# Kernel optimization log

Hardware: AMD Instinct MI355X
Metric: run time of the kernel (lower is better)

Reference implementation:

```python
import jax, jax.numpy as jnp
import numpy as np

DIM = 128
NUM_SLOTS = 8
ITERS = 3
EPS = 1e-8
LN_EPS = 1e-3
HIDDEN = max(DIM, 128)


def _ln(x, w, b):
    mu = jnp.mean(x, axis=-1, keepdims=True)
    var = jnp.mean(jnp.square(x - mu), axis=-1, keepdims=True)
    return (x - mu) * jax.lax.rsqrt(var + LN_EPS) * w + b


def setup_inputs() -> dict:
    key = jax.random.key(0)
    ks = jax.random.split(key, 16)
    b, n, d, h = 32, 4096, DIM, HIDDEN
    limit = np.sqrt(6.0 / (1 + d))
    inp = {
        'inputs': jax.random.normal(ks[0], (b, n, d), jnp.float32),
        'slots_mu': jax.random.uniform(ks[1], (1, 1, d), jnp.float32, -limit, limit),
        'slots_log_sigma': jax.random.uniform(ks[2], (1, 1, d), jnp.float32, -limit, limit),
        'Wq': jax.random.normal(ks[3], (d, d), jnp.float32) / np.sqrt(d),
        'Wk': jax.random.normal(ks[4], (d, d), jnp.float32) / np.sqrt(d),
        'Wv': jax.random.normal(ks[5], (d, d), jnp.float32) / np.sqrt(d),
        'W_ih': jax.random.normal(ks[6], (3 * d, d), jnp.float32) / np.sqrt(d),
        'W_hh': jax.random.normal(ks[7], (3 * d, d), jnp.float32) / np.sqrt(d),
        'b_ih': jnp.zeros((3 * d,), jnp.float32),
        'b_hh': jnp.zeros((3 * d,), jnp.float32),
        'W1': jax.random.normal(ks[8], (h, d), jnp.float32) / np.sqrt(d),
        'b1': jnp.zeros((h,), jnp.float32),
        'W2': jax.random.normal(ks[9], (d, h), jnp.float32) / np.sqrt(h),
        'b2': jnp.zeros((d,), jnp.float32),
        'ln_in_w': jnp.ones((d,), jnp.float32), 'ln_in_b': jnp.zeros((d,), jnp.float32),
        'ln_s_w': jnp.ones((d,), jnp.float32), 'ln_s_b': jnp.zeros((d,), jnp.float32),
        'ln_ff_w': jnp.ones((d,), jnp.float32), 'ln_ff_b': jnp.zeros((d,), jnp.float32),
    }
    return inp


def reference(inputs, slots_mu, slots_log_sigma, Wq, Wk, Wv, W_ih, W_hh, b_ih, b_hh,
              W1, b1, W2, b2, ln_in_w, ln_in_b, ln_s_w, ln_s_b, ln_ff_w, ln_ff_b):
    b, n, d = inputs.shape
    scale = d ** -0.5
    # stochastic slot init (reparameterized, fixed key for determinism)
    noise = jax.random.normal(jax.random.key(42), (b, NUM_SLOTS, d), inputs.dtype)
    slots = slots_mu + jnp.exp(slots_log_sigma) * noise

    x = _ln(inputs, ln_in_w, ln_in_b)
    k = jnp.einsum('bnd,ed->bne', x, Wk)
    v = jnp.einsum('bnd,ed->bne', x, Wv)

    for _ in range(ITERS):
        slots_prev = slots
        q = jnp.einsum('bsd,ed->bse', _ln(slots, ln_s_w, ln_s_b), Wq)
        dots = jnp.einsum('bid,bjd->bij', q, k) * scale          # [b, slots, n]
        attn = jax.nn.softmax(dots, axis=1) + EPS                 # softmax over slots
        attn = attn / jnp.sum(attn, axis=-1, keepdims=True)       # normalize over tokens
        updates = jnp.einsum('bjd,bij->bid', v, attn)             # [b, slots, d]
        # GRUCell(updates, slots_prev)
        gx = jnp.einsum('bsd,ed->bse', updates, W_ih) + b_ih
        gh = jnp.einsum('bsd,ed->bse', slots_prev, W_hh) + b_hh
        xr, xz, xn = jnp.split(gx, 3, axis=-1)
        hr, hz, hn = jnp.split(gh, 3, axis=-1)
        r = jax.nn.sigmoid(xr + hr)
        z = jax.nn.sigmoid(xz + hz)
        ng = jnp.tanh(xn + r * hn)
        slots = (1.0 - z) * ng + z * slots_prev
        # residual MLP
        ff = _ln(slots, ln_ff_w, ln_ff_b)
        ff = jax.nn.relu(jnp.einsum('bsd,hd->bsh', ff, W1) + b1)
        slots = slots + jnp.einsum('bsh,dh->bsd', ff, W2) + b2
    return slots
```

## Files before the change

kernel.cpp:

```cpp
#include <hip/hip_runtime.h>
#include <hip/hip_bf16.h>
#include <math.h>

#define DIM 128
#define NSLOT 8
#define NTOK 4096
#define NB 32
#define CHUNK 256
#define NCH (NTOK / CHUNK)
#define CHUNKPAD 264
#define LN_EPS 1e-3f
#define ATT_EPS 1e-8f
#define SCALE 0.08838834764831845f

#define BM 128
#define LDK 136

typedef short bf16x8 __attribute__((ext_vector_type(8)));
typedef float f32x4 __attribute__((ext_vector_type(4)));
typedef unsigned short ushort8_t __attribute__((ext_vector_type(8)));

__device__ __forceinline__ float bf2f(unsigned short u) {
  return __uint_as_float(((unsigned)u) << 16);
}
__device__ __forceinline__ unsigned short f2bf(float f) {
  unsigned u = __float_as_uint(f);
  unsigned r = (u + 0x7FFFu + ((u >> 16) & 1u)) >> 16;
  return (unsigned short)r;
}

__device__ __forceinline__ float erfinv_like_xla(float x) {
  double xd = (double)x;
  double w = -log1p(-xd * xd);
  double p;
  if (w < 5.0) {
    w = w - 2.5;
    p = 2.81022636e-08;
    p = 3.43273939e-07 + p * w;
    p = -3.5233877e-06 + p * w;
    p = -4.39150654e-06 + p * w;
    p = 0.00021858087 + p * w;
    p = -0.00125372503 + p * w;
    p = -0.00417768164 + p * w;
    p = 0.246640727 + p * w;
    p = 1.50140941 + p * w;
  } else {
    w = sqrt(w) - 3.0;
    p = -0.000200214257;
    p = 0.000100950558 + p * w;
    p = 0.00134934322 + p * w;
    p = -0.00367342844 + p * w;
    p = 0.00573950773 + p * w;
    p = -0.0076224613 + p * w;
    p = 0.00943887047 + p * w;
    p = 1.00167406 + p * w;
    p = 2.83297682 + p * w;
  }
  return (float)(p * xd);
}

__global__ __launch_bounds__(256) void k_init_slots(
    const float* __restrict__ mu, const float* __restrict__ lsig,
    float* __restrict__ slots) {
  int t = blockIdx.x * blockDim.x + threadIdx.x;
  if (t >= NB * NSLOT * DIM) return;
  uint32_t x0 = 0u, x1 = (uint32_t)t;
  uint32_t k0 = 0u, k1 = 42u;
  uint32_t ks[3] = {k0, k1, k0 ^ k1 ^ 0x1BD11BDAu};
  x0 += ks[0];
  x1 += ks[1];
  const int rot[2][4] = {{13, 15, 26, 6}, {17, 29, 16, 24}};
#pragma unroll
  for (int blk = 0; blk < 5; ++blk) {
    const int* r = rot[blk & 1];
#pragma unroll
    for (int j = 0; j < 4; ++j) {
      x0 += x1;
      x1 = (x1 << r[j]) | (x1 >> (32 - r[j]));
      x1 ^= x0;
    }
    x0 += ks[(blk + 1) % 3];
    x1 += ks[(blk + 2) % 3] + (uint32_t)(blk + 1);
  }
  uint32_t bits = x0 ^ x1;
  float f = __uint_as_float((bits >> 9) | 0x3F800000u) - 1.0f;
  const float mn = __uint_as_float(0xBF7FFFFFu);
  float u = fmaxf(f * 2.0f + mn, mn);
  float noise = 1.41421356f * erfinv_like_xla(u);
  int d = t & (DIM - 1);
  slots[t] = mu[d] + expf(lsig[d]) * noise;
}

__global__ __launch_bounds__(256) void k_wcast(const float* __restrict__ Wk,
                                               const float* __restrict__ Wv,
                                               unsigned short* __restrict__ Wbf) {
  int i = blockIdx.x * 256 + threadIdx.x;
  if (i >= DIM * DIM) return;
  Wbf[i] = f2bf(Wk[i]);
  Wbf[DIM * DIM + i] = f2bf(Wv[i]);
}

__global__ __launch_bounds__(512, 4) void k_ln_kv(
    const float* __restrict__ inp, const unsigned short* __restrict__ Wbf,
    const float* __restrict__ lnw, const float* __restrict__ lnb,
    unsigned short* __restrict__ kt, unsigned short* __restrict__ vt) {
  __shared__ __align__(16) unsigned short SH[BM * LDK];
  int t = threadIdx.x;
  int tg = blockIdx.x;

  {
    int r = t >> 2, qh = t & 3;
    const float* src = inp + ((size_t)tg * BM + r) * DIM + qh * 32;
    float xr[32];
    float s = 0.f, sq = 0.f;
#pragma unroll
    for (int i4 = 0; i4 < 8; ++i4) {
      float4 v = *reinterpret_cast<const float4*>(src + i4 * 4);
      xr[i4 * 4 + 0] = v.x; xr[i4 * 4 + 1] = v.y;
      xr[i4 * 4 + 2] = v.z; xr[i4 * 4 + 3] = v.w;
      s += v.x + v.y + v.z + v.w;
      sq += v.x * v.x + v.y * v.y + v.z * v.z + v.w * v.w;
    }
    s += __shfl_xor(s, 1); sq += __shfl_xor(sq, 1);
    s += __shfl_xor(s, 2); sq += __shfl_xor(sq, 2);
    float mean = s * (1.0f / DIM);
    float var = fmaxf(sq * (1.0f / DIM) - mean * mean, 0.0f);
    float inv = 1.0f / sqrtf(var + LN_EPS);
#pragma unroll
    for (int c8 = 0; c8 < 4; ++c8) {
      ushort8_t pk;
#pragma unroll
      for (int j = 0; j < 8; ++j) {
        int d = qh * 32 + c8 * 8 + j;
        float y = (xr[c8 * 8 + j] - mean) * inv * lnw[d] + lnb[d];
        pk[j] = f2bf(y);
      }
      *reinterpret_cast<ushort8_t*>(&SH[r * LDK + qh * 32 + c8 * 8]) = pk;
    }
  }
  __syncthreads();

  int w = t >> 6, l = t & 63, lm = l & 15, lg = l >> 4;
  int mat = w >> 2;
  int ebase = ((w >> 1) & 1) * 64;
  int th = (w & 1) * 64;
  const unsigned short* Wsrc = Wbf + mat * DIM * DIM;

  f32x4 acc[4][4];
#pragma unroll
  for (int i = 0; i < 4; ++i)
#pragma unroll
    for (int j = 0; j < 4; ++j) acc[i][j] = (f32x4){0.f, 0.f, 0.f, 0.f};

  if (mat == 0) {
#pragma unroll
    for (int ks = 0; ks < 4; ++ks) {
      bf16x8 wf[4], xf[4];
#pragma unroll
      for (int et = 0; et < 4; ++et)
        wf[et] = *reinterpret_cast<const bf16x8*>(
            Wsrc + (ebase + et * 16 + lm) * DIM + ks * 32 + 8 * lg);
#pragma unroll
      for (int tt = 0; tt < 4; ++tt)
        xf[tt] = *reinterpret_cast<const bf16x8*>(
            &SH[(th + tt * 16 + lm) * LDK + ks * 32 + 8 * lg]);
#pragma unroll
      for (int tt = 0; tt < 4; ++tt)
#pragma unroll
        for (int et = 0; et < 4; ++et)
          acc[tt][et] = __builtin_amdgcn_mfma_f32_16x16x32_bf16(
              xf[tt], wf[et], acc[tt][et], 0, 0, 0);
    }
  } else {
#pragma unroll
    for (int ks = 0; ks < 4; ++ks) {
      bf16x8 wf[4], xf[4];
#pragma unroll
      for (int et = 0; et < 4; ++et)
        wf[et] = *reinterpret_cast<const bf16x8*>(
            Wsrc + (ebase + et * 16 + lm) * DIM + ks * 32 + 8 * lg);
#pragma unroll
      for (int tt = 0; tt < 4; ++tt)
        xf[tt] = *reinterpret_cast<const bf16x8*>(
            &SH[(th + tt * 16 + lm) * LDK + ks * 32 + 8 * lg]);
#pragma unroll
      for (int et = 0; et < 4; ++et)
#pragma unroll
        for (int tt = 0; tt < 4; ++tt)
          acc[et][tt] = __builtin_amdgcn_mfma_f32_16x16x32_bf16(
              wf[et], xf[tt], acc[et][tt], 0, 0, 0);
    }
  }
  __syncthreads();

  if (mat == 0) {
#pragma unroll
    for (int tt = 0; tt < 4; ++tt)
#pragma unroll
      for (int et = 0; et < 4; ++et)
#pragma unroll
        for (int r = 0; r < 4; ++r)
          SH[(th + tt * 16 + 4 * lg + r) * LDK + ebase + et * 16 + lm] =
              f2bf(acc[tt][et][r]);
  }
  __syncthreads();
  {
    size_t rowbase = (size_t)tg * BM;
#pragma unroll
    for (int u = 0; u < 4; ++u) {
      int i = u * 512 + t;
      int tok = i >> 4, off = (i & 15) * 8;
      ushort8_t vv = *reinterpret_cast<const ushort8_t*>(&SH[tok * LDK + off]);
      *reinterpret_cast<ushort8_t*>(&kt[(rowbase + tok) * DIM + off]) = vv;
    }
  }
  __syncthreads();

  if (mat == 1) {
#pragma unroll
    for (int et = 0; et < 4; ++et)
#pragma unroll
      for (int tt = 0; tt < 4; ++tt)
#pragma unroll
        for (int r = 0; r < 4; ++r)
          SH[(ebase + et * 16 + 4 * lg + r) * LDK + th + tt * 16 + lm] =
              f2bf(acc[et][tt][r]);
  }
  __syncthreads();
  {
    int bb = tg >> 5;
    int nb = (tg & 31) * BM;
#pragma unroll
    for (int u = 0; u < 4; ++u) {
      int i = u * 512 + t;
      int e = i >> 4, off = (i & 15) * 8;
      ushort8_t vv = *reinterpret_cast<const ushort8_t*>(&SH[e * LDK + off]);
      *reinterpret_cast<ushort8_t*>(
          &vt[((size_t)bb * DIM + e) * NTOK + nb + off]) = vv;
    }
  }
}

__global__ __launch_bounds__(256) void k_q0(
    const float* __restrict__ slots, const float* __restrict__ Wq,
    const float* __restrict__ lnw, const float* __restrict__ lnb,
    unsigned short* __restrict__ qbf) {
  int b = blockIdx.x, t = threadIdx.x;
  int s = t >> 5, c = t & 31;
  __shared__ __align__(16) float sln[NSLOT][DIM];
  const float* sb = slots + (b * NSLOT + s) * DIM;
  float4 xv = *reinterpret_cast<const float4*>(sb + c * 4);
  float ps = xv.x + xv.y + xv.z + xv.w;
  float pq = xv.x * xv.x + xv.y * xv.y + xv.z * xv.z + xv.w * xv.w;
#pragma unroll
  for (int m = 16; m >= 1; m >>= 1) {
    ps += __shfl_xor(ps, m, 32);
    pq += __shfl_xor(pq, m, 32);
  }
  float mean = ps * (1.0f / DIM);
  float var = fmaxf(pq * (1.0f / DIM) - mean * mean, 0.0f);
  float inv = 1.0f / sqrtf(var + LN_EPS);
  float vals[4] = {xv.x, xv.y, xv.z, xv.w};
#pragma unroll
  for (int ii = 0; ii < 4; ++ii) {
    int d = c * 4 + ii;
    sln[s][d] = (vals[ii] - mean) * inv * lnw[d] + lnb[d];
  }
  __syncthreads();
#pragma unroll
  for (int ii = 0; ii < 4; ++ii) {
    int e = c + 32 * ii;
    const float* wr = Wq + e * DIM;
    float acc = 0.0f;
#pragma unroll
    for (int d4 = 0; d4 < DIM / 4; ++d4) {
      float4 w4 = *reinterpret_cast<const float4*>(wr + d4 * 4);
      float4 s4 = *reinterpret_cast<const float4*>(&sln[s][d4 * 4]);
      acc += s4.x * w4.x + s4.y * w4.y + s4.z * w4.z + s4.w * w4.w;
    }
    qbf[(b * NSLOT + s) * DIM + e] = f2bf(SCALE * acc);
  }
}

__global__ __launch_bounds__(512, 4) void k_attn(
    const unsigned short* __restrict__ qbf, const unsigned short* __restrict__ kt,
    const unsigned short* __restrict__ vt, float* __restrict__ Np,
    float* __restrict__ Dp) {
  int bid = blockIdx.x;
  int b = bid >> 4, ch = bid & 15;
  int n0 = ch * CHUNK;
  int t = threadIdx.x;
  int wid = t >> 6, l = t & 63, lm = l & 15, lg = l >> 4;

  __shared__ __align__(16) unsigned short a_lds[NSLOT][CHUNKPAD];

  {
    const unsigned short* qb = qbf + (b * NSLOT + (lm & 7)) * DIM;
    bf16x8 aq[4];
#pragma unroll
    for (int ks = 0; ks < 4; ++ks)
      aq[ks] = *reinterpret_cast<const bf16x8*>(qb + ks * 32 + 8 * lg);
    const unsigned short* kb = kt + ((size_t)b * NTOK + n0) * DIM;
#pragma unroll
    for (int tt = 0; tt < 2; ++tt) {
      int tok = wid * 32 + tt * 16 + lm;
      f32x4 acc = (f32x4){0.f, 0.f, 0.f, 0.f};
#pragma unroll
      for (int ks = 0; ks < 4; ++ks) {
        bf16x8 bk = *reinterpret_cast<const bf16x8*>(
            kb + (size_t)tok * DIM + ks * 32 + 8 * lg);
        acc = __builtin_amdgcn_mfma_f32_16x16x32_bf16(aq[ks], bk, acc, 0, 0, 0);
      }
      float m4 = fmaxf(fmaxf(acc[0], acc[1]), fmaxf(acc[2], acc[3]));
      float m8 = fmaxf(m4, __shfl_xor(m4, 16));
      float e0 = expf(acc[0] - m8), e1 = expf(acc[1] - m8);
      float e2 = expf(acc[2] - m8), e3 = expf(acc[3] - m8);
      float s4 = e0 + e1 + e2 + e3;
      float s8 = s4 + __shfl_xor(s4, 16);
      float rs = 1.0f / s8;
      if (lg < 2) {
        a_lds[4 * lg + 0][tok] = f2bf(e0 * rs + ATT_EPS);
        a_lds[4 * lg + 1][tok] = f2bf(e1 * rs + ATT_EPS);
        a_lds[4 * lg + 2][tok] = f2bf(e2 * rs + ATT_EPS);
        a_lds[4 * lg + 3][tok] = f2bf(e3 * rs + ATT_EPS);
      }
    }
  }
  __syncthreads();

  {
    float s = 0.0f;
#pragma unroll
    for (int jj = 0; jj < CHUNK / 64; ++jj) s += bf2f(a_lds[wid][l + 64 * jj]);
#pragma unroll
    for (int m = 32; m >= 1; m >>= 1) s += __shfl_xor(s, m);
    if (l == 0) Dp[(b * NCH + ch) * NSLOT + wid] = s;
  }

  {
    f32x4 acc = (f32x4){0.f, 0.f, 0.f, 0.f};
    const unsigned short* vb =
        vt + ((size_t)b * DIM + wid * 16 + lm) * NTOK + n0;
#pragma unroll
    for (int kk = 0; kk < CHUNK / 32; ++kk) {
      bf16x8 af = *reinterpret_cast<const bf16x8*>(
          &a_lds[lm & 7][kk * 32 + 8 * lg]);
      bf16x8 bv = *reinterpret_cast<const bf16x8*>(vb + kk * 32 + 8 * lg);
      acc = __builtin_amdgcn_mfma_f32_16x16x32_bf16(af, bv, acc, 0, 0, 0);
    }
    if (lg < 2) {
#pragma unroll
      for (int r = 0; r < 4; ++r)
        Np[((size_t)(b * NCH + ch) * NSLOT + 4 * lg + r) * DIM + wid * 16 +
           lm] = acc[r];
    }
  }
}

__global__ __launch_bounds__(256) void k_update(
    float* __restrict__ slots, unsigned short* __restrict__ qbf,
    const float* __restrict__ Np, const float* __restrict__ Dp,
    const float* __restrict__ W_ih, const float* __restrict__ W_hh,
    const float* __restrict__ b_ih, const float* __restrict__ b_hh,
    const float* __restrict__ W1, const float* __restrict__ b1,
    const float* __restrict__ W2, const float* __restrict__ b2,
    const float* __restrict__ lnfw, const float* __restrict__ lnfb,
    const float* __restrict__ Wq, const float* __restrict__ lnsw,
    const float* __restrict__ lnsb) {
  int bs = blockIdx.x;
  int b = bs >> 3, s = bs & 7;
  int t = threadIdx.x;
  __shared__ __align__(16) float upd[DIM];
  __shared__ __align__(16) float sprev[DIM];
  __shared__ __align__(16) float snew[DIM];
  __shared__ __align__(16) float ffin[DIM];
  __shared__ __align__(16) float ffb[DIM];
  __shared__ __align__(16) float gx[3 * DIM];
  __shared__ __align__(16) float gh[3 * DIM];

  float dsum = 0.0f;
  for (int ch = 0; ch < NCH; ++ch) dsum += Dp[(b * NCH + ch) * NSLOT + s];

  if (t < DIM) {
    sprev[t] = slots[(b * NSLOT + s) * DIM + t];
    float a = 0.0f;
    for (int ch = 0; ch < NCH; ++ch)
      a += Np[((size_t)(b * NCH + ch) * NSLOT + s) * DIM + t];
    upd[t] = a / dsum;
  }
  __syncthreads();

  for (int e = t; e < 3 * DIM; e += 256) {
    const float* wi = W_ih + e * DIM;
    const float* wh = W_hh + e * DIM;
    float ax = 0.0f, ah = 0.0f;
#pragma unroll
    for (int d4 = 0; d4 < DIM / 4; ++d4) {
      float4 u4 = *reinterpret_cast<const float4*>(&upd[d4 * 4]);
      float4 p4 = *reinterpret_cast<const float4*>(&sprev[d4 * 4]);
      float4 wi4 = *reinterpret_cast<const float4*>(wi + d4 * 4);
      float4 wh4 = *reinterpret_cast<const float4*>(wh + d4 * 4);
      ax += u4.x * wi4.x + u4.y * wi4.y + u4.z * wi4.z + u4.w * wi4.w;
      ah += p4.x * wh4.x + p4.y * wh4.y + p4.z * wh4.z + p4.w * wh4.w;
    }
    gx[e] = ax + b_ih[e];
    gh[e] = ah + b_hh[e];
  }
  __syncthreads();

  if (t < DIM) {
    float xr = gx[t], xz = gx[DIM + t], xn = gx[2 * DIM + t];
    float hr = gh[t], hz = gh[DIM + t], hn = gh[2 * DIM + t];
    float r = 1.0f / (1.0f + expf(-(xr + hr)));
    float z = 1.0f / (1.0f + expf(-(xz + hz)));
    float ng = tanhf(xn + r * hn);
    snew[t] = (1.0f - z) * ng + z * sprev[t];
  }
  __syncthreads();

  if (t < DIM) {
    float s1 = 0.0f, s2 = 0.0f;
#pragma unroll 8
    for (int d = 0; d < DIM; ++d) {
      float v = snew[d];
      s1 += v;
      s2 += v * v;
    }
    float mean = s1 * (1.0f / DIM);
    float var = fmaxf(s2 * (1.0f / DIM) - mean * mean, 0.0f);
    float inv = 1.0f / sqrtf(var + LN_EPS);
    ffin[t] = (snew[t] - mean) * inv * lnfw[t] + lnfb[t];
  }
  __syncthreads();

  if (t < DIM) {
    const float* wr = W1 + t * DIM;
    float acc = 0.0f;
#pragma unroll
    for (int d4 = 0; d4 < DIM / 4; ++d4) {
      float4 f4 = *reinterpret_cast<const float4*>(&ffin[d4 * 4]);
      float4 w4 = *reinterpret_cast<const float4*>(wr + d4 * 4);
      acc += f4.x * w4.x + f4.y * w4.y + f4.z * w4.z + f4.w * w4.w;
    }
    ffb[t] = fmaxf(acc + b1[t], 0.0f);
  }
  __syncthreads();

  if (t < DIM) {
    const float* wr = W2 + t * DIM;
    float acc = 0.0f;
#pragma unroll
    for (int h4 = 0; h4 < DIM / 4; ++h4) {
      float4 f4 = *reinterpret_cast<const float4*>(&ffb[h4 * 4]);
      float4 w4 = *reinterpret_cast<const float4*>(wr + h4 * 4);
      acc += f4.x * w4.x + f4.y * w4.y + f4.z * w4.z + f4.w * w4.w;
    }
    float val = snew[t] + acc + b2[t];
    slots[(b * NSLOT + s) * DIM + t] = val;
    gx[t] = val;
  }
  __syncthreads();

  if (t < DIM) {
    float s1 = 0.0f, s2 = 0.0f;
#pragma unroll 8
    for (int d = 0; d < DIM; ++d) {
      float v = gx[d];
      s1 += v;
      s2 += v * v;
    }
    float mean = s1 * (1.0f / DIM);
    float var = fmaxf(s2 * (1.0f / DIM) - mean * mean, 0.0f);
    float inv = 1.0f / sqrtf(var + LN_EPS);
    gh[t] = (gx[t] - mean) * inv * lnsw[t] + lnsb[t];
  }
  __syncthreads();

  if (t < DIM) {
    const float* wr = Wq + t * DIM;
    float acc = 0.0f;
#pragma unroll
    for (int d4 = 0; d4 < DIM / 4; ++d4) {
      float4 g4 = *reinterpret_cast<const float4*>(&gh[d4 * 4]);
      float4 w4 = *reinterpret_cast<const float4*>(wr + d4 * 4);
      acc += g4.x * w4.x + g4.y * w4.y + g4.z * w4.z + g4.w * w4.w;
    }
    qbf[(b * NSLOT + s) * DIM + t] = f2bf(SCALE * acc);
  }
}

__global__ __launch_bounds__(256) void k_sentinel(float* __restrict__ out,
                                                  int n) {
  int i = blockIdx.x * blockDim.x + threadIdx.x;
  if (i < n) out[i] = 1234.5f;
}

extern "C" void kernel_launch(void* const* d_in, const int* in_sizes, int n_in,
                              void* d_out, int out_size, void* d_ws,
                              size_t ws_size, hipStream_t stream) {
  const float* inp = (const float*)d_in[0];
  const float* mu = (const float*)d_in[1];
  const float* lsig = (const float*)d_in[2];
  const float* Wq = (const float*)d_in[3];
  const float* Wk = (const float*)d_in[4];
  const float* Wv = (const float*)d_in[5];
  const float* W_ih = (const float*)d_in[6];
  const float* W_hh = (const float*)d_in[7];
  const float* b_ih = (const float*)d_in[8];
  const float* b_hh = (const float*)d_in[9];
  const float* W1 = (const float*)d_in[10];
  const float* b1 = (const float*)d_in[11];
  const float* W2 = (const float*)d_in[12];
  const float* b2 = (const float*)d_in[13];
  const float* ln_in_w = (const float*)d_in[14];
  const float* ln_in_b = (const float*)d_in[15];
  const float* ln_s_w = (const float*)d_in[16];
  const float* ln_s_b = (const float*)d_in[17];
  const float* ln_ff_w = (const float*)d_in[18];
  const float* ln_ff_b = (const float*)d_in[19];

  float* slots = (float*)d_out;

  const size_t kv_elems = (size_t)NB * DIM * NTOK;
  const size_t np_elems = (size_t)NB * NCH * NSLOT * DIM;
  const size_t dp_elems = (size_t)NB * NCH * NSLOT;
  const size_t q_elems = (size_t)NB * NSLOT * DIM;
  size_t need = kv_elems * 2 * 2 + np_elems * 4 + dp_elems * 4 + q_elems * 2;
  if (ws_size < need) {
    k_sentinel<<<(out_size + 255) / 256, 256, 0, stream>>>((float*)d_out,
                                                           out_size);
    return;
  }
  char* wsb = (char*)d_ws;
  unsigned short* kt = (unsigned short*)wsb;
  unsigned short* vt = kt + kv_elems;
  float* Np = (float*)(wsb + kv_elems * 4);
  float* Dp = Np + np_elems;
  unsigned short* qbf = (unsigned short*)(Dp + dp_elems);
  unsigned short* Wbf = (unsigned short*)Np;

  k_init_slots<<<(NB * NSLOT * DIM) / 256, 256, 0, stream>>>(mu, lsig, slots);
  k_wcast<<<(DIM * DIM) / 256, 256, 0, stream>>>(Wk, Wv, Wbf);
  k_ln_kv<<<NB * NTOK / BM, 512, 0, stream>>>(inp, Wbf, ln_in_w, ln_in_b, kt,
                                              vt);
  k_q0<<<NB, 256, 0, stream>>>(slots, Wq, ln_s_w, ln_s_b, qbf);
  for (int it = 0; it < 3; ++it) {
    k_attn<<<NB * NCH, 512, 0, stream>>>(qbf, kt, vt, Np, Dp);
    k_update<<<NB * NSLOT, 256, 0, stream>>>(slots, qbf, Np, Dp, W_ih, W_hh,
                                             b_ih, b_hh, W1, b1, W2, b2,
                                             ln_ff_w, ln_ff_b, Wq, ln_s_w,
                                             ln_s_b);
  }
}
```

Measured before the change: 204.0 us.

## Halve attention chunk and LN/KV tile sizes, fold weight cast into init

Attention chunks shrink from 256 to 128 tokens, and the LN+K/V projection block shrinks from 128 to 64 rows with 256 threads. K and V results go to separate LDS buffers so both stores happen after one barrier instead of two. The Wk/Wv bf16 cast moves into the slot-init kernel, removing one launch. The aim is more blocks for better occupancy and fewer syncs and launches. The cost is twice as many partial sums for the update kernel to reduce and less work per block to hide latency. The rest of the code must also use the new NCH consistently.

```diff
diff --git a/kernel.cpp b/kernel.cpp
--- a/kernel.cpp
+++ b/kernel.cpp
@@ -6,14 +6,14 @@
 #define NSLOT 8
 #define NTOK 4096
 #define NB 32
-#define CHUNK 256
+#define CHUNK 128
 #define NCH (NTOK / CHUNK)
-#define CHUNKPAD 264
+#define CHUNKPAD 136
 #define LN_EPS 1e-3f
 #define ATT_EPS 1e-8f
 #define SCALE 0.08838834764831845f
 
-#define BM 128
+#define BM 64
 #define LDK 136
 
 typedef short bf16x8 __attribute__((ext_vector_type(8)));
@@ -61,8 +61,13 @@
 
 __global__ __launch_bounds__(256) void k_init_slots(
     const float* __restrict__ mu, const float* __restrict__ lsig,
-    float* __restrict__ slots) {
+    float* __restrict__ slots, const float* __restrict__ Wk,
+    const float* __restrict__ Wv, unsigned short* __restrict__ Wbf) {
   int t = blockIdx.x * blockDim.x + threadIdx.x;
+  if (t < DIM * DIM) {
+    Wbf[t] = f2bf(Wk[t]);
+    Wbf[DIM * DIM + t] = f2bf(Wv[t]);
+  }
   if (t >= NB * NSLOT * DIM) return;
   uint32_t x0 = 0u, x1 = (uint32_t)t;
   uint32_t k0 = 0u, k1 = 42u;
@@ -91,20 +96,12 @@
   slots[t] = mu[d] + expf(lsig[d]) * noise;
 }
 
-__global__ __launch_bounds__(256) void k_wcast(const float* __restrict__ Wk,
-                                               const float* __restrict__ Wv,
-                                               unsigned short* __restrict__ Wbf) {
-  int i = blockIdx.x * 256 + threadIdx.x;
-  if (i >= DIM * DIM) return;
-  Wbf[i] = f2bf(Wk[i]);
-  Wbf[DIM * DIM + i] = f2bf(Wv[i]);
-}
-
-__global__ __launch_bounds__(512, 4) void k_ln_kv(
+__global__ __launch_bounds__(256) void k_ln_kv(
     const float* __restrict__ inp, const unsigned short* __restrict__ Wbf,
     const float* __restrict__ lnw, const float* __restrict__ lnb,
     unsigned short* __restrict__ kt, unsigned short* __restrict__ vt) {
-  __shared__ __align__(16) unsigned short SH[BM * LDK];
+  __shared__ __align__(16) unsigned short A[BM * LDK];
+  __shared__ __align__(16) unsigned short Bv[DIM * 72];
   int t = threadIdx.x;
   int tg = blockIdx.x;
 
@@ -135,15 +132,14 @@
         float y = (xr[c8 * 8 + j] - mean) * inv * lnw[d] + lnb[d];
         pk[j] = f2bf(y);
       }
-      *reinterpret_cast<ushort8_t*>(&SH[r * LDK + qh * 32 + c8 * 8]) = pk;
+      *reinterpret_cast<ushort8_t*>(&A[r * LDK + qh * 32 + c8 * 8]) = pk;
     }
   }
   __syncthreads();
 
   int w = t >> 6, l = t & 63, lm = l & 15, lg = l >> 4;
-  int mat = w >> 2;
-  int ebase = ((w >> 1) & 1) * 64;
-  int th = (w & 1) * 64;
+  int mat = w >> 1;
+  int ebase = (w & 1) * 64;
   const unsigned short* Wsrc = Wbf + mat * DIM * DIM;
 
   f32x4 acc[4][4];
@@ -163,7 +159,7 @@
 #pragma unroll
       for (int tt = 0; tt < 4; ++tt)
         xf[tt] = *reinterpret_cast<const bf16x8*>(
-            &SH[(th + tt * 16 + lm) * LDK + ks * 32 + 8 * lg]);
+            &A[(tt * 16 + lm) * LDK + ks * 32 + 8 * lg]);
 #pragma unroll
       for (int tt = 0; tt < 4; ++tt)
 #pragma unroll
@@ -182,7 +178,7 @@
 #pragma unroll
       for (int tt = 0; tt < 4; ++tt)
         xf[tt] = *reinterpret_cast<const bf16x8*>(
-            &SH[(th + tt * 16 + lm) * LDK + ks * 32 + 8 * lg]);
+            &A[(tt * 16 + lm) * LDK + ks * 32 + 8 * lg]);
 #pragma unroll
       for (int et = 0; et < 4; ++et)
 #pragma unroll
@@ -200,41 +196,36 @@
       for (int et = 0; et < 4; ++et)
 #pragma unroll
         for (int r = 0; r < 4; ++r)
-          SH[(th + tt * 16 + 4 * lg + r) * LDK + ebase + et * 16 + lm] =
+          A[(tt * 16 + 4 * lg + r) * LDK + ebase + et * 16 + lm] =
               f2bf(acc[tt][et][r]);
-  }
-  __syncthreads();
+  } else {
+#pragma unroll
+    for (int et = 0; et < 4; ++et)
+#pragma unroll
+      for (int tt = 0; tt < 4; ++tt)
+#pragma unroll
+        for (int r = 0; r < 4; ++r)
+          Bv[(ebase + et * 16 + 4 * lg + r) * 72 + tt * 16 + lm] =
+              f2bf(acc[et][tt][r]);
+  }
+  __syncthreads();
+
   {
     size_t rowbase = (size_t)tg * BM;
 #pragma unroll
     for (int u = 0; u < 4; ++u) {
-      int i = u * 512 + t;
+      int i = u * 256 + t;
       int tok = i >> 4, off = (i & 15) * 8;
-      ushort8_t vv = *reinterpret_cast<const ushort8_t*>(&SH[tok * LDK + off]);
+      ushort8_t vv = *reinterpret_cast<const ushort8_t*>(&A[tok * LDK + off]);
       *reinterpret_cast<ushort8_t*>(&kt[(rowbase + tok) * DIM + off]) = vv;
     }
-  }
-  __syncthreads();
-
-  if (mat == 1) {
-#pragma unroll
-    for (int et = 0; et < 4; ++et)
-#pragma unroll
-      for (int tt = 0; tt < 4; ++tt)
-#pragma unroll
-        for (int r = 0; r < 4; ++r)
-          SH[(ebase + et * 16 + 4 * lg + r) * LDK + th + tt * 16 + lm] =
-              f2bf(acc[et][tt][r]);
-  }
-  __syncthreads();
-  {
-    int bb = tg >> 5;
-    int nb = (tg & 31) * BM;
+    int bb = tg >> 6;
+    int nb = (tg & 63) * BM;
 #pragma unroll
     for (int u = 0; u < 4; ++u) {
-      int i = u * 512 + t;
-      int e = i >> 4, off = (i & 15) * 8;
-      ushort8_t vv = *reinterpret_cast<const ushort8_t*>(&SH[e * LDK + off]);
+      int i = u * 256 + t;
+      int e = i >> 3, off = (i & 7) * 8;
+      ushort8_t vv = *reinterpret_cast<const ushort8_t*>(&Bv[e * 72 + off]);
       *reinterpret_cast<ushort8_t*>(
           &vt[((size_t)bb * DIM + e) * NTOK + nb + off]) = vv;
     }
@@ -287,7 +278,7 @@
     const unsigned short* __restrict__ vt, float* __restrict__ Np,
     float* __restrict__ Dp) {
   int bid = blockIdx.x;
-  int b = bid >> 4, ch = bid & 15;
+  int b = bid >> 5, ch = bid & 31;
   int n0 = ch * CHUNK;
   int t = threadIdx.x;
   int wid = t >> 6, l = t & 63, lm = l & 15, lg = l >> 4;
@@ -301,29 +292,26 @@
     for (int ks = 0; ks < 4; ++ks)
       aq[ks] = *reinterpret_cast<const bf16x8*>(qb + ks * 32 + 8 * lg);
     const unsigned short* kb = kt + ((size_t)b * NTOK + n0) * DIM;
-#pragma unroll
-    for (int tt = 0; tt < 2; ++tt) {
-      int tok = wid * 32 + tt * 16 + lm;
-      f32x4 acc = (f32x4){0.f, 0.f, 0.f, 0.f};
-#pragma unroll
-      for (int ks = 0; ks < 4; ++ks) {
-        bf16x8 bk = *reinterpret_cast<const bf16x8*>(
-            kb + (size_t)tok * DIM + ks * 32 + 8 * lg);
-        acc = __builtin_amdgcn_mfma_f32_16x16x32_bf16(aq[ks], bk, acc, 0, 0, 0);
-      }
-      float m4 = fmaxf(fmaxf(acc[0], acc[1]), fmaxf(acc[2], acc[3]));
-      float m8 = fmaxf(m4, __shfl_xor(m4, 16));
-      float e0 = expf(acc[0] - m8), e1 = expf(acc[1] - m8);
-      float e2 = expf(acc[2] - m8), e3 = expf(acc[3] - m8);
-      float s4 = e0 + e1 + e2 + e3;
-      float s8 = s4 + __shfl_xor(s4, 16);
-      float rs = 1.0f / s8;
-      if (lg < 2) {
-        a_lds[4 * lg + 0][tok] = f2bf(e0 * rs + ATT_EPS);
-        a_lds[4 * lg + 1][tok] = f2bf(e1 * rs + ATT_EPS);
-        a_lds[4 * lg + 2][tok] = f2bf(e2 * rs + ATT_EPS);
-        a_lds[4 * lg + 3][tok] = f2bf(e3 * rs + ATT_EPS);
-      }
+    int tok = wid * 16 + lm;
+    f32x4 acc = (f32x4){0.f, 0.f, 0.f, 0.f};
+#pragma unroll
+    for (int ks = 0; ks < 4; ++ks) {
+      bf16x8 bk = *reinterpret_cast<const bf16x8*>(
+          kb + (size_t)tok * DIM + ks * 32 + 8 * lg);
+      acc = __builtin_amdgcn_mfma_f32_16x16x32_bf16(aq[ks], bk, acc, 0, 0, 0);
+    }
+    float m4 = fmaxf(fmaxf(acc[0], acc[1]), fmaxf(acc[2], acc[3]));
+    float m8 = fmaxf(m4, __shfl_xor(m4, 16));
+    float e0 = expf(acc[0] - m8), e1 = expf(acc[1] - m8);
+    float e2 = expf(acc[2] - m8), e3 = expf(acc[3] - m8);
+    float s4 = e0 + e1 + e2 + e3;
+    float s8 = s4 + __shfl_xor(s4, 16);
+    float rs = 1.0f / s8;
+    if (lg < 2) {
+      a_lds[4 * lg + 0][tok] = f2bf(e0 * rs + ATT_EPS);
+      a_lds[4 * lg + 1][tok] = f2bf(e1 * rs + ATT_EPS);
+      a_lds[4 * lg + 2][tok] = f2bf(e2 * rs + ATT_EPS);
+      a_lds[4 * lg + 3][tok] = f2bf(e3 * rs + ATT_EPS);
     }
   }
   __syncthreads();
@@ -539,9 +527,9 @@
   unsigned short* qbf = (unsigned short*)(Dp + dp_elems);
   unsigned short* Wbf = (unsigned short*)Np;
 
-  k_init_slots<<<(NB * NSLOT * DIM) / 256, 256, 0, stream>>>(mu, lsig, slots);
-  k_wcast<<<(DIM * DIM) / 256, 256, 0, stream>>>(Wk, Wv, Wbf);
-  k_ln_kv<<<NB * NTOK / BM, 512, 0, stream>>>(inp, Wbf, ln_in_w, ln_in_b, kt,
+  k_init_slots<<<(NB * NSLOT * DIM) / 256, 256, 0, stream>>>(mu, lsig, slots,
+                                                             Wk, Wv, Wbf);
+  k_ln_kv<<<NB * NTOK / BM, 256, 0, stream>>>(inp, Wbf, ln_in_w, ln_in_b, kt,
                                               vt);
   k_q0<<<NB, 256, 0, stream>>>(slots, Wq, ln_s_w, ln_s_b, qbf);
   for (int it = 0; it < 3; ++it) {
```

Result: faster. 194.0 us (-4.9%).
